# Kernel tuning notes

Measured on AMD Instinct MI355X. Metric: run time of the kernel, lower is better.

Reference implementation:

```python
import jax, jax.numpy as jnp
import numpy as np

B, IN, H1, H2, OUT, P = 8192, 1024, 2048, 2048, 1024, 8


def setup_inputs() -> dict:
    key = jax.random.key(0)
    ks = jax.random.split(key, 12)
    s = 0.02
    return {
        "x": jax.random.normal(ks[0], (B, IN), dtype=jnp.float32),
        # layer 1: P expert linears (stacked) + selector
        "W1": jax.random.normal(ks[1], (P, IN, H1), dtype=jnp.float32) * s,
        "b1": jax.random.normal(ks[2], (P, H1), dtype=jnp.float32) * s,
        "S1": jax.random.normal(ks[3], (IN, P), dtype=jnp.float32) * s,
        "sb1": jax.random.normal(ks[4], (P,), dtype=jnp.float32) * s,
        # layer 2
        "W2": jax.random.normal(ks[5], (P, H1, H2), dtype=jnp.float32) * s,
        "b2": jax.random.normal(ks[6], (P, H2), dtype=jnp.float32) * s,
        "S2": jax.random.normal(ks[7], (H1, P), dtype=jnp.float32) * s,
        "sb2": jax.random.normal(ks[8], (P,), dtype=jnp.float32) * s,
        # classifier
        "Wc": jax.random.normal(ks[9], (H2, OUT), dtype=jnp.float32) * s,
        "bc": jax.random.normal(ks[10], (OUT,), dtype=jnp.float32) * s,
    }


def _drn_layer(x, W, b, S, sb):
    # selector + softmax routing probs: [B, P]
    probs = jax.nn.softmax(x @ S + sb, axis=-1)
    # all-expert dense outputs: [B, P, O]
    outs = jnp.einsum('bi,pio->bpo', x, W) + b[None, :, :]
    # soft-weighted combine over experts
    return jnp.einsum('bpo,bp->bo', outs, probs)


def reference(x, W1, b1, S1, sb1, W2, b2, S2, sb2, Wc, bc):
    h = jax.nn.relu(_drn_layer(x, W1, b1, S1, sb1))
    h = jax.nn.relu(_drn_layer(h, W2, b2, S2, sb2))
    return h @ Wc + bc
```

## Files before the change

kernel.cpp:

```cpp
#include <hip/hip_runtime.h>
#include <hip/hip_bf16.h>

#define B_SZ   8192
#define IN_SZ  1024
#define H1_SZ  2048
#define H2_SZ  2048
#define OUT_SZ 1024
#define NP     8

typedef __bf16 bf16x8 __attribute__((ext_vector_type(8)));
typedef float  f32x4  __attribute__((ext_vector_type(4)));

__device__ __forceinline__ void async_ld16(const void* g, void* l) {
    __builtin_amdgcn_global_load_lds(
        (const __attribute__((address_space(1))) unsigned int*)g,
        (__attribute__((address_space(3))) unsigned int*)l,
        16, 0, 0);
}

__device__ __forceinline__ void transpose_body(float (*tile)[33],
                                               const float* __restrict__ in,
                                               __hip_bfloat16* __restrict__ out,
                                               int K, int N, int bx, int by) {
    int n0 = bx * 32, k0 = by * 32;
    int tx = threadIdx.x, ty = threadIdx.y;
#pragma unroll
    for (int j = 0; j < 4; ++j)
        tile[ty + j * 8][tx] = in[(size_t)(k0 + ty + j * 8) * N + (n0 + tx)];
    __syncthreads();
    const int kk = (tx & 15) * 2;
#pragma unroll
    for (int j = 0; j < 2; ++j) {
        int nn = ty + j * 8 + (tx >> 4) * 16;
        __hip_bfloat16 t2[2] = {__float2bfloat16(tile[kk][nn]),
                                __float2bfloat16(tile[kk + 1][nn])};
        unsigned int u;
        __builtin_memcpy(&u, t2, 4);
        *(unsigned int*)(out + (size_t)(n0 + nn) * K + (k0 + kk)) = u;
    }
}

__global__ void prep_k(const float* __restrict__ W1, const float* __restrict__ W2,
                       const float* __restrict__ Wc, const float* __restrict__ x,
                       __hip_bfloat16* __restrict__ W1t, __hip_bfloat16* __restrict__ W2t,
                       __hip_bfloat16* __restrict__ Wct, __hip_bfloat16* __restrict__ xbf) {
    __shared__ float tile[32][33];
    int id = blockIdx.x;
    const int nA = (H1_SZ / 32) * ((NP * IN_SZ) / 32);
    const int nB = (H2_SZ / 32) * ((NP * H1_SZ) / 32);
    const int nC = (OUT_SZ / 32) * (H2_SZ / 32);
    if (id < nA) {
        transpose_body(tile, W1, W1t, NP * IN_SZ, H1_SZ, id % (H1_SZ / 32), id / (H1_SZ / 32));
        return;
    }
    id -= nA;
    if (id < nB) {
        transpose_body(tile, W2, W2t, NP * H1_SZ, H2_SZ, id % (H2_SZ / 32), id / (H2_SZ / 32));
        return;
    }
    id -= nB;
    if (id < nC) {
        transpose_body(tile, Wc, Wct, H2_SZ, OUT_SZ, id % (OUT_SZ / 32), id / (OUT_SZ / 32));
        return;
    }
    id -= nC;
    {
        int t = threadIdx.y * 32 + threadIdx.x;
        size_t i = ((size_t)id * 256 + t) * 8;
        float4 f0 = *(const float4*)(x + i);
        float4 f1 = *(const float4*)(x + i + 4);
        __hip_bfloat16 tt[8] = {
            __float2bfloat16(f0.x), __float2bfloat16(f0.y),
            __float2bfloat16(f0.z), __float2bfloat16(f0.w),
            __float2bfloat16(f1.x), __float2bfloat16(f1.y),
            __float2bfloat16(f1.z), __float2bfloat16(f1.w)};
        uint4 u4;
        __builtin_memcpy(&u4, tt, 16);
        *(uint4*)(xbf + i) = u4;
    }
}

template <typename T>
__global__ void selector_k(const T* __restrict__ in, const float* __restrict__ S,
                           const float* __restrict__ sb, float* __restrict__ probs,
                           float* __restrict__ ratT, int K) {
    int row  = blockIdx.x * blockDim.y + threadIdx.y;
    int lane = threadIdx.x;
    float acc[NP];
#pragma unroll
    for (int p = 0; p < NP; ++p) acc[p] = 0.f;
    const T* xr = in + (size_t)row * K;
    for (int k = lane; k < K; k += 64) {
        float xv;
        if constexpr (sizeof(T) == 2) xv = __bfloat162float(xr[k]);
        else                          xv = (float)xr[k];
        const float* sr = S + (size_t)k * NP;
#pragma unroll
        for (int p = 0; p < NP; ++p) acc[p] += xv * sr[p];
    }
#pragma unroll
    for (int p = 0; p < NP; ++p)
#pragma unroll
        for (int off = 32; off > 0; off >>= 1)
            acc[p] += __shfl_down(acc[p], off, 64);
    if (lane == 0) {
        float v[NP], m = -1e30f;
#pragma unroll
        for (int p = 0; p < NP; ++p) { v[p] = acc[p] + sb[p]; m = fmaxf(m, v[p]); }
        float s = 0.f;
#pragma unroll
        for (int p = 0; p < NP; ++p) { v[p] = expf(v[p] - m); s += v[p]; }
        float inv = 1.f / s;
#pragma unroll
        for (int p = 0; p < NP; ++p) probs[(size_t)row * NP + p] = v[p] * inv;
#pragma unroll
        for (int p = 0; p < NP - 1; ++p) ratT[(size_t)p * B_SZ + row] = v[p] / v[p + 1];
        ratT[(size_t)(NP - 1) * B_SZ + row] = v[NP - 1] * inv;
    }
}

template <int TPS>
__global__ __launch_bounds__(512, 2)
void drn_gemm8_k(const __hip_bfloat16* __restrict__ A, const __hip_bfloat16* __restrict__ Wt,
                 int N, int K, int Kin, const float* __restrict__ ratT,
                 const float* __restrict__ probs, const float* __restrict__ bexp,
                 __hip_bfloat16* __restrict__ C) {
    __shared__ alignas(16) char smem[131072];

    const int tid  = threadIdx.x;
    const int wid  = tid >> 6, lane = tid & 63;
    const int quad = lane >> 4, l16 = lane & 15;
    const int wr = wid >> 2, wc = wid & 3;

    const int g   = blockIdx.x;
    const int cpx = gridDim.x >> 3;
    const int wg  = (g & 7) * cpx + (g >> 3);
    const int nbn = N >> 8;
    const int mb  = wg / nbn, nb = wg % nbn;
    const int m0  = mb * 256, n0 = nb * 256;

    const int arow = tid >> 3;
    const int gsw  = ((tid & 7) ^ (arow & 7)) << 3;
    const __hip_bfloat16* Ag = A  + (size_t)(m0 + arow) * Kin + gsw;
    const __hip_bfloat16* Bg = Wt + (size_t)(n0 + arow) * K + gsw;
    const size_t r64a = (size_t)64 * Kin;
    const size_t r64b = (size_t)64 * K;
    char* aDst = smem + wid * 1024;
    char* bDst = smem + 65536 + wid * 1024;

#define STG_A(dbuf, ksrc, h) do {                                              \
    const __hip_bfloat16* s_ = Ag + (((ksrc) & (TPS - 1)) * 64) + (size_t)(2*(h)) * r64a; \
    char* d_ = aDst + (dbuf) * 32768 + (h) * 16384;                            \
    async_ld16(s_,        d_);                                                 \
    async_ld16(s_ + r64a, d_ + 8192); } while (0)
#define STG_B(dbuf, ksrc, h) do {                                              \
    const __hip_bfloat16* s_ = Bg + ((size_t)(ksrc) * 64) + (size_t)(2*(h)) * r64b; \
    char* d_ = bDst + (dbuf) * 32768 + (h) * 16384;                            \
    async_ld16(s_,        d_);                                                 \
    async_ld16(s_ + r64b, d_ + 8192); } while (0)

    const int csw   = (quad ^ (l16 & 7)) << 4;
    const int abase = (wr * 128 + l16) * 128 + csw;
    const int bbase = 65536 + (wc * 64 + l16) * 128 + csw;
    const char* aB[2][2] = {{smem + abase,         smem + (abase ^ 64)},
                            {smem + 32768 + abase, smem + 32768 + (abase ^ 64)}};
    const char* bB[2][2] = {{smem + bbase,         smem + (bbase ^ 64)},
                            {smem + 32768 + bbase, smem + 32768 + (bbase ^ 64)}};

#define LD_A4(d, mh, kh)                                                        \
    af[0] = *(const bf16x8*)(aB[d][kh] + ((mh) * 4 + 0) * 2048);                \
    af[1] = *(const bf16x8*)(aB[d][kh] + ((mh) * 4 + 1) * 2048);                \
    af[2] = *(const bf16x8*)(aB[d][kh] + ((mh) * 4 + 2) * 2048);                \
    af[3] = *(const bf16x8*)(aB[d][kh] + ((mh) * 4 + 3) * 2048)
#define LD_B4(d, kh)                                                            \
    bfr[0][kh] = *(const bf16x8*)(bB[d][kh] + 0 * 2048);                        \
    bfr[1][kh] = *(const bf16x8*)(bB[d][kh] + 1 * 2048);                        \
    bfr[2][kh] = *(const bf16x8*)(bB[d][kh] + 2 * 2048);                        \
    bfr[3][kh] = *(const bf16x8*)(bB[d][kh] + 3 * 2048)

#define BAR()                                              \
    __builtin_amdgcn_s_barrier();                          \
    __builtin_amdgcn_sched_barrier(0)

#define LGKM0()                                            \
    asm volatile("s_waitcnt lgkmcnt(0)" ::: "memory");     \
    __builtin_amdgcn_sched_barrier(0)

#define VMW(n) asm volatile("s_waitcnt vmcnt(" #n ")" ::: "memory")

#define MF(mh, kh) do {                                    \
    __builtin_amdgcn_s_setprio(1);                         \
    _Pragma("unroll")                                      \
    for (int ml = 0; ml < 4; ++ml)                         \
      _Pragma("unroll")                                    \
      for (int n_ = 0; n_ < 4; ++n_)                       \
        acc[(mh) * 4 + ml][n_] = __builtin_amdgcn_mfma_f32_16x16x32_bf16( \
            af[ml], bfr[n_][kh], acc[(mh) * 4 + ml][n_], 0, 0, 0);        \
    __builtin_amdgcn_s_setprio(0); } while (0)

    f32x4 zero = {0.f, 0.f, 0.f, 0.f};
    f32x4 acc[8][4];
#pragma unroll
    for (int m = 0; m < 8; ++m)
#pragma unroll
        for (int n = 0; n < 4; ++n) acc[m][n] = zero;

    const int NT = K >> 6;
    const int NI = NT >> 1;

    STG_A(0, 0, 0); STG_A(0, 0, 1);
    STG_B(0, 0, 0); STG_B(0, 0, 1);
    STG_B(1, 1, 0); STG_B(1, 1, 1);
    VMW(4);
    BAR();

    bf16x8 af[4], bfr[4][2];

    for (int i = 0; i < NI; ++i) {
        const int T  = 2 * i;
        const int k2 = (T + 2 < NT) ? T + 2 : NT - 1;
        const int k3 = (T + 3 < NT) ? T + 3 : NT - 1;

        STG_A(1, T + 1, 0); LD_B4(0, 0); LD_A4(0, 0, 0);
        BAR(); LGKM0(); MF(0, 0); BAR();
        STG_A(1, T + 1, 1); LD_B4(0, 1); LD_A4(0, 0, 1);
        BAR(); LGKM0(); MF(0, 1); BAR();
        STG_B(0, k2, 0);                 LD_A4(0, 1, 0);
        BAR(); LGKM0(); MF(1, 0); BAR();
        STG_B(0, k2, 1);                 LD_A4(0, 1, 1);
        BAR(); LGKM0(); MF(1, 1);
        VMW(4); BAR();

        STG_A(0, k2, 0); LD_B4(1, 0); LD_A4(1, 0, 0);
        BAR(); LGKM0(); MF(0, 0); BAR();
        STG_A(0, k2, 1); LD_B4(1, 1); LD_A4(1, 0, 1);
        BAR(); LGKM0(); MF(0, 1); BAR();
        STG_B(1, k3, 0);              LD_A4(1, 1, 0);
        BAR(); LGKM0(); MF(1, 0); BAR();
        STG_B(1, k3, 1);              LD_A4(1, 1, 1);
        BAR(); LGKM0(); MF(1, 1);
        VMW(4); BAR();

        if (((i + 1) & (TPS / 2 - 1)) == 0) {
            const int p = (i + 1) / (TPS / 2) - 1;
            const float* rp = ratT + (size_t)p * B_SZ + (m0 + wr * 128 + quad * 4);
            f32x4 rr[8];
#pragma unroll
            for (int m = 0; m < 8; ++m) rr[m] = *(const f32x4*)(rp + m * 16);
#pragma unroll
            for (int m = 0; m < 8; ++m)
#pragma unroll
                for (int n = 0; n < 4; ++n)
                    acc[m][n] *= rr[m];
        }
    }

    asm volatile("s_waitcnt vmcnt(0)" ::: "memory");

    const int colb = n0 + wc * 64 + l16;
    float bx[4][NP];
#pragma unroll
    for (int n = 0; n < 4; ++n)
#pragma unroll
        for (int p = 0; p < NP; ++p)
            bx[n][p] = bexp[(size_t)p * N + colb + n * 16];
#pragma unroll
    for (int m = 0; m < 8; ++m) {
#pragma unroll
        for (int r = 0; r < 4; ++r) {
            const int row = m0 + wr * 128 + m * 16 + quad * 4 + r;
            const float* pr = probs + (size_t)row * NP;
            f32x4 p0 = *(const f32x4*)pr;
            f32x4 p1 = *(const f32x4*)(pr + 4);
            float pv[NP] = {p0[0], p0[1], p0[2], p0[3], p1[0], p1[1], p1[2], p1[3]};
#pragma unroll
            for (int n = 0; n < 4; ++n) {
                float bsum = 0.f;
#pragma unroll
                for (int p = 0; p < NP; ++p) bsum += pv[p] * bx[n][p];
                float v = fmaxf(acc[m][n][r] + bsum, 0.f);
                C[(size_t)row * N + colb + n * 16] = __float2bfloat16(v);
            }
        }
    }
#undef STG_A
#undef STG_B
#undef LD_A4
#undef LD_B4
#undef BAR
#undef LGKM0
#undef VMW
#undef MF
}

__global__ __launch_bounds__(256)
void gemm_bt_k(const __hip_bfloat16* __restrict__ A, const __hip_bfloat16* __restrict__ Bt,
               int M, int N, int K, const float* __restrict__ bias, float* __restrict__ C) {
    __shared__ alignas(16) __hip_bfloat16 As[2 * 128 * 32];
    __shared__ alignas(16) __hip_bfloat16 Bs[2 * 128 * 32];
    const int tid  = threadIdx.x;
    const int wid  = tid >> 6, lane = tid & 63;
    const int quad = lane >> 4, l16 = lane & 15;
    const int waveM = (wid >> 1) << 6, waveN = (wid & 1) << 6;
    const int m0 = blockIdx.x * 128, n0 = blockIdx.y * 128;

    f32x4 zero = {0.f, 0.f, 0.f, 0.f};
    f32x4 acc[4][4];
#pragma unroll
    for (int a = 0; a < 4; ++a)
#pragma unroll
        for (int b = 0; b < 4; ++b) acc[a][b] = zero;

    const int srow = tid >> 2;
    const int skc  = (((tid & 3) ^ (srow & 3) ^ ((srow >> 2) & 3)) << 3);
    const __hip_bfloat16* Ag = A  + (size_t)(m0 + srow) * K + skc;
    const __hip_bfloat16* Bg = Bt + (size_t)(n0 + srow) * K + skc;
    const size_t rowStep = (size_t)64 * K;
    __hip_bfloat16* AsB = As + wid * 512;
    __hip_bfloat16* BsB = Bs + wid * 512;
    const int csel = (quad ^ (l16 & 3) ^ ((l16 >> 2) & 3)) << 3;

    async_ld16(Ag,           AsB);
    async_ld16(Ag + rowStep, AsB + 2048);
    async_ld16(Bg,           BsB);
    async_ld16(Bg + rowStep, BsB + 2048);

    for (int kt = 0; kt < K; kt += 32) {
        const int cur = (kt >> 5) & 1;
        __syncthreads();
        if (kt + 32 < K) {
            const int nb = (1 - cur) * 4096;
            async_ld16(Ag + kt + 32,           AsB + nb);
            async_ld16(Ag + kt + 32 + rowStep, AsB + nb + 2048);
            async_ld16(Bg + kt + 32,           BsB + nb);
            async_ld16(Bg + kt + 32 + rowStep, BsB + nb + 2048);
        }
        const __hip_bfloat16* AsC = As + cur * 4096;
        const __hip_bfloat16* BsC = Bs + cur * 4096;
        bf16x8 af[4], bfr[4];
#pragma unroll
        for (int q = 0; q < 4; ++q) {
            af[q]  = *(const bf16x8*)(AsC + (waveM + q * 16 + l16) * 32 + csel);
            bfr[q] = *(const bf16x8*)(BsC + (waveN + q * 16 + l16) * 32 + csel);
        }
#pragma unroll
        for (int tm = 0; tm < 4; ++tm)
#pragma unroll
            for (int tn = 0; tn < 4; ++tn)
                acc[tm][tn] = __builtin_amdgcn_mfma_f32_16x16x32_bf16(
                    af[tm], bfr[tn], acc[tm][tn], 0, 0, 0);
    }

    const int colb = n0 + waveN + l16;
#pragma unroll
    for (int tm = 0; tm < 4; ++tm)
#pragma unroll
        for (int r = 0; r < 4; ++r) {
            int row = m0 + waveM + tm * 16 + quad * 4 + r;
#pragma unroll
            for (int tn = 0; tn < 4; ++tn)
                C[(size_t)row * N + colb + tn * 16] =
                    acc[tm][tn][r] + bias[colb + tn * 16];
        }
}

extern "C" void kernel_launch(void* const* d_in, const int* in_sizes, int n_in,
                              void* d_out, int out_size, void* d_ws, size_t ws_size,
                              hipStream_t stream) {
    const float* x   = (const float*)d_in[0];
    const float* W1  = (const float*)d_in[1];
    const float* b1  = (const float*)d_in[2];
    const float* S1  = (const float*)d_in[3];
    const float* sb1 = (const float*)d_in[4];
    const float* W2  = (const float*)d_in[5];
    const float* b2  = (const float*)d_in[6];
    const float* S2  = (const float*)d_in[7];
    const float* sb2 = (const float*)d_in[8];
    const float* Wc  = (const float*)d_in[9];
    const float* bc  = (const float*)d_in[10];
    float* out = (float*)d_out;

    char* ws = (char*)d_ws;
    size_t off = 0;
    auto alloc = [&](size_t bytes) {
        char* p = ws + off;
        off += (bytes + 255) & ~(size_t)255;
        return p;
    };
    __hip_bfloat16* W1t = (__hip_bfloat16*)alloc((size_t)H1_SZ * (NP * IN_SZ) * 2);
    __hip_bfloat16* W2t = (__hip_bfloat16*)alloc((size_t)H2_SZ * (NP * H1_SZ) * 2);
    __hip_bfloat16* Wct = (__hip_bfloat16*)alloc((size_t)OUT_SZ * H2_SZ * 2);
    float* probs1       = (float*)alloc((size_t)B_SZ * NP * 4);
    float* probs2       = (float*)alloc((size_t)B_SZ * NP * 4);
    float* rat1         = (float*)alloc((size_t)NP * B_SZ * 4);
    float* rat2         = (float*)alloc((size_t)NP * B_SZ * 4);
    __hip_bfloat16* xbf = (__hip_bfloat16*)alloc((size_t)B_SZ * IN_SZ * 2);
    __hip_bfloat16* h1  = (__hip_bfloat16*)alloc((size_t)B_SZ * H1_SZ * 2);
    __hip_bfloat16* h2  = (__hip_bfloat16*)alloc((size_t)B_SZ * H2_SZ * 2);

    const int nPrep = (H1_SZ / 32) * ((NP * IN_SZ) / 32)
                    + (H2_SZ / 32) * ((NP * H1_SZ) / 32)
                    + (OUT_SZ / 32) * (H2_SZ / 32)
                    + (B_SZ * IN_SZ) / (256 * 8);
    prep_k<<<nPrep, dim3(32, 8), 0, stream>>>(W1, W2, Wc, x, W1t, W2t, Wct, xbf);

    selector_k<float><<<B_SZ / 4, dim3(64, 4), 0, stream>>>(x, S1, sb1, probs1, rat1, IN_SZ);
    drn_gemm8_k<16><<<(B_SZ / 256) * (H1_SZ / 256), 512, 0, stream>>>(
        xbf, W1t, H1_SZ, NP * IN_SZ, IN_SZ, rat1, probs1, b1, h1);

    selector_k<__hip_bfloat16><<<B_SZ / 4, dim3(64, 4), 0, stream>>>(h1, S2, sb2, probs2, rat2, H1_SZ);
    drn_gemm8_k<32><<<(B_SZ / 256) * (H2_SZ / 256), 512, 0, stream>>>(
        h1, W2t, H2_SZ, NP * H1_SZ, H1_SZ, rat2, probs2, b2, h2);

    gemm_bt_k<<<dim3(B_SZ / 128, OUT_SZ / 128), 256, 0, stream>>>(
        h2, Wct, B_SZ, OUT_SZ, H2_SZ, bc, out);
}
```

Before: 995.3 us.

## Load B operand directly from global into registers, bypassing LDS staging

The weight (B) tiles are no longer staged through shared memory with async global-to-LDS copies. Each wave now reads its B fragments straight from global memory into registers, double-buffered in two register sets. This halves the LDS footprint, which removes the LDS traffic for B and may allow more workgroups per CU. In exchange, B data shared by the two wave rows is fetched twice, the row-strided global loads are poorly coalesced, and compiler-inserted vmcnt waits may stall the MFMA stream. The final prefetch also reads past the end of K.

```diff
diff --git a/kernel.cpp b/kernel.cpp
--- a/kernel.cpp
+++ b/kernel.cpp
@@ -125,7 +125,7 @@
                  int N, int K, int Kin, const float* __restrict__ ratT,
                  const float* __restrict__ probs, const float* __restrict__ bexp,
                  __hip_bfloat16* __restrict__ C) {
-    __shared__ alignas(16) char smem[131072];
+    __shared__ alignas(16) char smem[65536];
 
     const int tid  = threadIdx.x;
     const int wid  = tid >> 6, lane = tid & 63;
@@ -141,42 +141,42 @@
 
     const int arow = tid >> 3;
     const int gsw  = ((tid & 7) ^ (arow & 7)) << 3;
-    const __hip_bfloat16* Ag = A  + (size_t)(m0 + arow) * Kin + gsw;
-    const __hip_bfloat16* Bg = Wt + (size_t)(n0 + arow) * K + gsw;
+    const __hip_bfloat16* Ag = A + (size_t)(m0 + arow) * Kin + gsw;
     const size_t r64a = (size_t)64 * Kin;
-    const size_t r64b = (size_t)64 * K;
     char* aDst = smem + wid * 1024;
-    char* bDst = smem + 65536 + wid * 1024;
 
 #define STG_A(dbuf, ksrc, h) do {                                              \
     const __hip_bfloat16* s_ = Ag + (((ksrc) & (TPS - 1)) * 64) + (size_t)(2*(h)) * r64a; \
     char* d_ = aDst + (dbuf) * 32768 + (h) * 16384;                            \
     async_ld16(s_,        d_);                                                 \
     async_ld16(s_ + r64a, d_ + 8192); } while (0)
-#define STG_B(dbuf, ksrc, h) do {                                              \
-    const __hip_bfloat16* s_ = Bg + ((size_t)(ksrc) * 64) + (size_t)(2*(h)) * r64b; \
-    char* d_ = bDst + (dbuf) * 32768 + (h) * 16384;                            \
-    async_ld16(s_,        d_);                                                 \
-    async_ld16(s_ + r64b, d_ + 8192); } while (0)
 
     const int csw   = (quad ^ (l16 & 7)) << 4;
     const int abase = (wr * 128 + l16) * 128 + csw;
-    const int bbase = 65536 + (wc * 64 + l16) * 128 + csw;
     const char* aB[2][2] = {{smem + abase,         smem + (abase ^ 64)},
                             {smem + 32768 + abase, smem + 32768 + (abase ^ 64)}};
-    const char* bB[2][2] = {{smem + bbase,         smem + (bbase ^ 64)},
-                            {smem + 32768 + bbase, smem + 32768 + (bbase ^ 64)}};
 
 #define LD_A4(d, mh, kh)                                                        \
     af[0] = *(const bf16x8*)(aB[d][kh] + ((mh) * 4 + 0) * 2048);                \
     af[1] = *(const bf16x8*)(aB[d][kh] + ((mh) * 4 + 1) * 2048);                \
     af[2] = *(const bf16x8*)(aB[d][kh] + ((mh) * 4 + 2) * 2048);                \
     af[3] = *(const bf16x8*)(aB[d][kh] + ((mh) * 4 + 3) * 2048)
-#define LD_B4(d, kh)                                                            \
-    bfr[0][kh] = *(const bf16x8*)(bB[d][kh] + 0 * 2048);                        \
-    bfr[1][kh] = *(const bf16x8*)(bB[d][kh] + 1 * 2048);                        \
-    bfr[2][kh] = *(const bf16x8*)(bB[d][kh] + 2 * 2048);                        \
-    bfr[3][kh] = *(const bf16x8*)(bB[d][kh] + 3 * 2048)
+
+    const __hip_bfloat16* bp0 = Wt + (size_t)(n0 + wc * 64 +  0 + l16) * K + quad * 8;
+    const __hip_bfloat16* bp1 = Wt + (size_t)(n0 + wc * 64 + 16 + l16) * K + quad * 8;
+    const __hip_bfloat16* bp2 = Wt + (size_t)(n0 + wc * 64 + 32 + l16) * K + quad * 8;
+    const __hip_bfloat16* bp3 = Wt + (size_t)(n0 + wc * 64 + 48 + l16) * K + quad * 8;
+
+#define LD_BX(off)                                        \
+    bX[0] = *(const bf16x8*)(bp0 + (off));                \
+    bX[1] = *(const bf16x8*)(bp1 + (off));                \
+    bX[2] = *(const bf16x8*)(bp2 + (off));                \
+    bX[3] = *(const bf16x8*)(bp3 + (off))
+#define LD_BY(off)                                        \
+    bY[0] = *(const bf16x8*)(bp0 + (off));                \
+    bY[1] = *(const bf16x8*)(bp1 + (off));                \
+    bY[2] = *(const bf16x8*)(bp2 + (off));                \
+    bY[3] = *(const bf16x8*)(bp3 + (off))
 
 #define BAR()                                              \
     __builtin_amdgcn_s_barrier();                          \
@@ -188,14 +188,14 @@
 
 #define VMW(n) asm volatile("s_waitcnt vmcnt(" #n ")" ::: "memory")
 
-#define MF(mh, kh) do {                                    \
+#define MF(mh, bArr) do {                                  \
     __builtin_amdgcn_s_setprio(1);                         \
     _Pragma("unroll")                                      \
     for (int ml = 0; ml < 4; ++ml)                         \
       _Pragma("unroll")                                    \
       for (int n_ = 0; n_ < 4; ++n_)                       \
         acc[(mh) * 4 + ml][n_] = __builtin_amdgcn_mfma_f32_16x16x32_bf16( \
-            af[ml], bfr[n_][kh], acc[(mh) * 4 + ml][n_], 0, 0, 0);        \
+            af[ml], bArr[n_], acc[(mh) * 4 + ml][n_], 0, 0, 0);           \
     __builtin_amdgcn_s_setprio(0); } while (0)
 
     f32x4 zero = {0.f, 0.f, 0.f, 0.f};
@@ -208,38 +208,46 @@
     const int NT = K >> 6;
     const int NI = NT >> 1;
 
+    bf16x8 af[4], bX[4], bY[4];
+
     STG_A(0, 0, 0); STG_A(0, 0, 1);
-    STG_B(0, 0, 0); STG_B(0, 0, 1);
-    STG_B(1, 1, 0); STG_B(1, 1, 1);
+    LD_BX(0);
     VMW(4);
     BAR();
-
-    bf16x8 af[4], bfr[4][2];
 
     for (int i = 0; i < NI; ++i) {
         const int T  = 2 * i;
         const int k2 = (T + 2 < NT) ? T + 2 : NT - 1;
-        const int k3 = (T + 3 < NT) ? T + 3 : NT - 1;
-
-        STG_A(1, T + 1, 0); LD_B4(0, 0); LD_A4(0, 0, 0);
-        BAR(); LGKM0(); MF(0, 0); BAR();
-        STG_A(1, T + 1, 1); LD_B4(0, 1); LD_A4(0, 0, 1);
-        BAR(); LGKM0(); MF(0, 1); BAR();
-        STG_B(0, k2, 0);                 LD_A4(0, 1, 0);
-        BAR(); LGKM0(); MF(1, 0); BAR();
-        STG_B(0, k2, 1);                 LD_A4(0, 1, 1);
-        BAR(); LGKM0(); MF(1, 1);
+
+        STG_A(1, T + 1, 0);
+        LD_BY(32);
+        LD_A4(0, 0, 0);
+        BAR(); LGKM0(); MF(0, bX); BAR();
+        STG_A(1, T + 1, 1);
+        LD_A4(0, 1, 0);
+        BAR(); LGKM0(); MF(1, bX); BAR();
+        LD_BX(64);
+        LD_A4(0, 0, 1);
+        BAR(); LGKM0(); MF(0, bY); BAR();
+        LD_A4(0, 1, 1);
+        BAR(); LGKM0(); MF(1, bY);
         VMW(4); BAR();
-
-        STG_A(0, k2, 0); LD_B4(1, 0); LD_A4(1, 0, 0);
-        BAR(); LGKM0(); MF(0, 0); BAR();
-        STG_A(0, k2, 1); LD_B4(1, 1); LD_A4(1, 0, 1);
-        BAR(); LGKM0(); MF(0, 1); BAR();
-        STG_B(1, k3, 0);              LD_A4(1, 1, 0);
-        BAR(); LGKM0(); MF(1, 0); BAR();
-        STG_B(1, k3, 1);              LD_A4(1, 1, 1);
-        BAR(); LGKM0(); MF(1, 1);
+        bp0 += 64; bp1 += 64; bp2 += 64; bp3 += 64;
+
+        STG_A(0, k2, 0);
+        LD_BY(32);
+        LD_A4(1, 0, 0);
+        BAR(); LGKM0(); MF(0, bX); BAR();
+        STG_A(0, k2, 1);
+        LD_A4(1, 1, 0);
+        BAR(); LGKM0(); MF(1, bX); BAR();
+        LD_BX(64);
+        LD_A4(1, 0, 1);
+        BAR(); LGKM0(); MF(0, bY); BAR();
+        LD_A4(1, 1, 1);
+        BAR(); LGKM0(); MF(1, bY);
         VMW(4); BAR();
+        bp0 += 64; bp1 += 64; bp2 += 64; bp3 += 64;
 
         if (((i + 1) & (TPS / 2 - 1)) == 0) {
             const int p = (i + 1) / (TPS / 2) - 1;
@@ -284,9 +292,9 @@
         }
     }
 #undef STG_A
-#undef STG_B
 #undef LD_A4
-#undef LD_B4
+#undef LD_BX
+#undef LD_BY
 #undef BAR
 #undef LGKM0
 #undef VMW
```

Result: slower. 1.444 ms (+45.1%).
